# Performance work log

Hardware: AMD Instinct MI355X
Metric: run time of the kernel (lower is better)

## Reference

```python
import jax, jax.numpy as jnp
import numpy as np

D_MODEL = 1024
N_HEADS = 16
SEQ = 2048
BATCH = 2


def setup_inputs() -> dict:
    key = jax.random.key(0)
    ks = jax.random.split(key, 12)
    s = 1.0 / np.sqrt(D_MODEL)
    return {
        "q_input": jax.random.normal(ks[0], (BATCH, SEQ, D_MODEL), jnp.float32),
        "k_input": jax.random.normal(ks[1], (BATCH, SEQ, D_MODEL), jnp.float32),
        "v_input": jax.random.normal(ks[2], (BATCH, SEQ, D_MODEL), jnp.float32),
        "key_padding_mask": jnp.zeros((BATCH, SEQ), dtype=bool),
        "wq": jax.random.normal(ks[3], (D_MODEL, D_MODEL), jnp.float32) * s,
        "bq": jnp.zeros((D_MODEL,), jnp.float32),
        "wk": jax.random.normal(ks[4], (D_MODEL, D_MODEL), jnp.float32) * s,
        "bk": jnp.zeros((D_MODEL,), jnp.float32),
        "wv": jax.random.normal(ks[5], (D_MODEL, D_MODEL), jnp.float32) * s,
        "bv": jnp.zeros((D_MODEL,), jnp.float32),
        "wo": jax.random.normal(ks[6], (D_MODEL, D_MODEL), jnp.float32) * s,
        "bo": jnp.zeros((D_MODEL,), jnp.float32),
    }


def reference(q_input, k_input, v_input, key_padding_mask, wq, bq, wk, bk, wv, bv, wo, bo):
    B, Lq, _ = q_input.shape
    Lk = k_input.shape[1]
    d_head = D_MODEL // N_HEADS
    # torch Linear: x @ W.T + b
    Q = q_input @ wq.T + bq
    K = k_input @ wk.T + bk
    V = v_input @ wv.T + bv
    # [B, H, L, d_head]
    Qh = Q.reshape(B, Lq, N_HEADS, d_head).transpose(0, 2, 1, 3)
    Kh = K.reshape(B, Lk, N_HEADS, d_head).transpose(0, 2, 1, 3)
    Vh = V.reshape(B, Lk, N_HEADS, d_head).transpose(0, 2, 1, 3)
    scores = jnp.einsum("bhqd,bhkd->bhqk", Qh, Kh) / jnp.sqrt(jnp.float32(d_head))
    # causal mask (use_mask=True)
    causal = jnp.arange(Lk)[None, :] > jnp.arange(Lq)[:, None]  # [Lq, Lk]
    scores = jnp.where(causal[None, None], -jnp.inf, scores)
    # key padding mask [B,1,1,Lk]
    scores = jnp.where(key_padding_mask[:, None, None, :], -jnp.inf, scores)
    # module's global all-inf fallback (scalar condition)
    probs = jnp.where(
        jnp.all(jnp.isinf(scores)),
        jnp.full_like(scores, 1.0 / Lk),
        jax.nn.softmax(scores, axis=-1),
    )
    # dropout is identity in eval mode
    out = jnp.einsum("bhqk,bhkd->bhqd", probs, Vh)
    out = out.transpose(0, 2, 1, 3).reshape(B, Lq, D_MODEL)
    return out @ wo.T + bo
```

## Files before the change

kernel.cpp:

```cpp
#include <hip/hip_runtime.h>
#include <cstdint>
#include <cstddef>

#define DM   1024
#define HEADS 16
#define DH    64
#define SEQL  2048
#define BATCH 2
#define MTOT  (BATCH*SEQL)

typedef __attribute__((ext_vector_type(8))) short short8;
typedef __attribute__((ext_vector_type(4))) float floatx4;

__device__ __forceinline__ unsigned short f2bf(float f) {
  unsigned int u = __float_as_uint(f);
  u = (u + 0x7FFFu + ((u >> 16) & 1u)) >> 16;
  return (unsigned short)u;
}

__device__ __forceinline__ float exp2_fast(float x) {
#if __has_builtin(__builtin_amdgcn_exp2f)
  return __builtin_amdgcn_exp2f(x);
#else
  return exp2f(x);
#endif
}

__device__ __forceinline__ unsigned int cvt_pk_bf16(float lo, float hi) {
  unsigned int r;
  asm("v_cvt_pk_bf16_f32 %0, %1, %2" : "=v"(r) : "v"(lo), "v"(hi));
  return r;
}

__device__ __forceinline__ void async_ld16(const void* g, void* l) {
  __builtin_amdgcn_global_load_lds(
      (const __attribute__((address_space(1))) unsigned int*)g,
      (__attribute__((address_space(3))) unsigned int*)l, 16, 0, 0);
}

#define QSCALE 0.1803368801111204f

__global__ void cvt_all(const float* __restrict__ q, const float* __restrict__ k,
                        const float* __restrict__ v, const float* __restrict__ w0,
                        const float* __restrict__ w1, const float* __restrict__ w2,
                        const float* __restrict__ w3,
                        unsigned short* __restrict__ Xq, unsigned short* __restrict__ Xk,
                        unsigned short* __restrict__ Xv, unsigned short* __restrict__ W0,
                        unsigned short* __restrict__ W1, unsigned short* __restrict__ W2,
                        unsigned short* __restrict__ W3) {
  const int bid = blockIdx.x;
  const float* src; unsigned short* dst; int base;
  if (bid < 12288) {
    int seg = bid >> 12;
    base = (bid & 4095) * 1024;
    src = seg == 0 ? q : seg == 1 ? k : v;
    dst = seg == 0 ? Xq : seg == 1 ? Xk : Xv;
  } else {
    int b2 = bid - 12288;
    int seg = b2 >> 10;
    base = (b2 & 1023) * 1024;
    src = seg == 0 ? w0 : seg == 1 ? w1 : seg == 2 ? w2 : w3;
    dst = seg == 0 ? W0 : seg == 1 ? W1 : seg == 2 ? W2 : W3;
  }
  int i = base + threadIdx.x * 4;
  float4 vv = *(const float4*)(src + i);
  ushort4 o;
  o.x = f2bf(vv.x); o.y = f2bf(vv.y); o.z = f2bf(vv.z); o.w = f2bf(vv.w);
  *(ushort4*)(dst + i) = o;
}

__global__ __launch_bounds__(256, 3) void qkv_gemm(
    const unsigned short* Xq, const unsigned short* Xk, const unsigned short* Xv,
    const unsigned short* Wq, const unsigned short* Wk, const unsigned short* Wv,
    const float* bq, const float* bk, const float* bv,
    unsigned short* Qo, unsigned short* Ko, unsigned short* VTo) {
  __shared__ unsigned short As[128 * 64], Bs[128 * 64];
  const unsigned short *A, *Bw; const float* bias; unsigned short* Cout;
  if (blockIdx.z == 0)      { A = Xq; Bw = Wq; bias = bq; Cout = Qo; }
  else if (blockIdx.z == 1) { A = Xk; Bw = Wk; bias = bk; Cout = Ko; }
  else                      { A = Xv; Bw = Wv; bias = bv; Cout = VTo; }

  const int K = DM, N = DM;
  const int m0 = blockIdx.y * 128, n0 = blockIdx.x * 128;
  const int tid  = threadIdx.x;
  const int lane = tid & 63, wvi = tid >> 6;
  const int lq = lane & 15, quad = lane >> 4;
  const int wrow = wvi >> 1, wcol = wvi & 1;

  floatx4 acc[4][4];
  #pragma unroll
  for (int i = 0; i < 4; i++)
    #pragma unroll
    for (int j = 0; j < 4; j++)
      #pragma unroll
      for (int e = 0; e < 4; e++) acc[i][j][e] = 0.0f;

  for (int kt = 0; kt < K; kt += 64) {
    #pragma unroll
    for (int cc = 0; cc < 4; cc++) {
      int c = wvi + cc * 4;
      int e = c * 512 + lane * 8;
      int r = e >> 6, col = e & 63;
      async_ld16(A  + (size_t)(m0 + r) * K + kt + col, As + c * 512);
      async_ld16(Bw + (size_t)(n0 + r) * K + kt + col, Bs + c * 512);
    }
    __syncthreads();
    #pragma unroll
    for (int ks = 0; ks < 64; ks += 32) {
      short8 af[4], bf[4];
      #pragma unroll
      for (int i = 0; i < 4; i++)
        af[i] = *(const short8*)&As[(wrow * 64 + i * 16 + lq) * 64 + ks + quad * 8];
      #pragma unroll
      for (int j = 0; j < 4; j++)
        bf[j] = *(const short8*)&Bs[(wcol * 64 + j * 16 + lq) * 64 + ks + quad * 8];
      #pragma unroll
      for (int i = 0; i < 4; i++)
        #pragma unroll
        for (int j = 0; j < 4; j++)
          acc[i][j] = __builtin_amdgcn_mfma_f32_16x16x32_bf16(af[i], bf[j], acc[i][j], 0, 0, 0);
    }
    __syncthreads();
  }

  if (blockIdx.z == 2) {
    #pragma unroll
    for (int i = 0; i < 4; i++) {
      const int rowg = m0 + wrow * 64 + i * 16 + quad * 4;
      const int bb  = rowg >> 11;
      const int kt2 = (rowg & 2047) >> 6;
      const int k0  = rowg & 63;
      #pragma unroll
      for (int j = 0; j < 4; j++) {
        const int colg = n0 + wcol * 64 + j * 16 + lq;
        const int h2 = colg >> 6, d2 = colg & 63;
        const float bb_v = bias[colg];
        ushort4 w;
        w.x = f2bf(acc[i][j][0] + bb_v);
        w.y = f2bf(acc[i][j][1] + bb_v);
        w.z = f2bf(acc[i][j][2] + bb_v);
        w.w = f2bf(acc[i][j][3] + bb_v);
        *(ushort4*)(Cout + (size_t)((bb * HEADS + h2) * 32 + kt2) * 4096 + d2 * 64 + k0) = w;
      }
    }
  } else {
    const float oscale = (blockIdx.z == 0) ? QSCALE : 1.0f;
    #pragma unroll
    for (int i = 0; i < 4; i++) {
      #pragma unroll
      for (int j = 0; j < 4; j++) {
        int colg = n0 + wcol * 64 + j * 16 + lq;
        float bb = bias[colg];
        #pragma unroll
        for (int r = 0; r < 4; r++) {
          int rowg = m0 + wrow * 64 + i * 16 + quad * 4 + r;
          Cout[(size_t)rowg * N + colg] = f2bf((acc[i][j][r] + bb) * oscale);
        }
      }
    }
  }
}

__global__ __launch_bounds__(256, 4) void out_gemm(
    const unsigned short* __restrict__ A, const unsigned short* __restrict__ Bw,
    const float* __restrict__ bias, float* __restrict__ C) {
  __shared__ unsigned short As[64 * 64], Bs[128 * 64];
  const int K = DM, N = DM;
  const int m0 = blockIdx.y * 64, n0 = blockIdx.x * 128;
  const int tid  = threadIdx.x;
  const int lane = tid & 63, wvi = tid >> 6;
  const int lq = lane & 15, quad = lane >> 4;

  floatx4 acc[8];
  #pragma unroll
  for (int j = 0; j < 8; j++)
    #pragma unroll
    for (int e = 0; e < 4; e++) acc[j][e] = 0.0f;

  for (int kt = 0; kt < K; kt += 64) {
    #pragma unroll
    for (int cc = 0; cc < 2; cc++) {
      int c = wvi + cc * 4;
      int e = c * 512 + lane * 8;
      int r = e >> 6, col = e & 63;
      async_ld16(A + (size_t)(m0 + r) * K + kt + col, As + c * 512);
    }
    #pragma unroll
    for (int cc = 0; cc < 4; cc++) {
      int c = wvi + cc * 4;
      int e = c * 512 + lane * 8;
      int r = e >> 6, col = e & 63;
      async_ld16(Bw + (size_t)(n0 + r) * K + kt + col, Bs + c * 512);
    }
    __syncthreads();
    #pragma unroll
    for (int ks = 0; ks < 64; ks += 32) {
      const short8 af = *(const short8*)&As[(wvi * 16 + lq) * 64 + ks + quad * 8];
      #pragma unroll
      for (int j = 0; j < 8; j++) {
        const short8 bf = *(const short8*)&Bs[(j * 16 + lq) * 64 + ks + quad * 8];
        acc[j] = __builtin_amdgcn_mfma_f32_16x16x32_bf16(af, bf, acc[j], 0, 0, 0);
      }
    }
    __syncthreads();
  }

  #pragma unroll
  for (int j = 0; j < 8; j++) {
    const int colg = n0 + j * 16 + lq;
    const float bb = bias[colg];
    #pragma unroll
    for (int r = 0; r < 4; r++) {
      const int rowg = m0 + wvi * 16 + quad * 4 + r;
      C[(size_t)rowg * N + colg] = acc[j][r] + bb;
    }
  }
}

__global__ __launch_bounds__(256, 4) void attn_kernel(
    const unsigned short* __restrict__ Q, const unsigned short* __restrict__ K,
    const unsigned short* __restrict__ VT, const unsigned char* __restrict__ kpm,
    unsigned short* __restrict__ O) {
  __shared__ unsigned short Ks[64 * 72];
  __shared__ unsigned short VTs[64 * 72];
  __shared__ unsigned short Ps[4][16 * 72];

  const int bid = blockIdx.x;
  const int qt = 31 - (bid >> 5);
  const int bh = bid & 31;
  const int h = bh & 15, b = bh >> 4;
  const int tid = threadIdx.x, lane = tid & 63, wvi = tid >> 6;
  const int lq = lane & 15, quad = lane >> 4;
  const size_t bbase = (size_t)b * SEQL * DM;

  const int srow = tid >> 4;
  const int scol = (tid & 15) * 4;

  const unsigned short* kptr = K + bbase + (size_t)h * DH + (size_t)srow * DM + scol;
  const unsigned short* vptr = VT + (size_t)(b * HEADS + h) * 32 * 4096 + srow * 64 + scol;
  const unsigned char*  mptr = kpm + (size_t)b * SEQL + quad * 4;

  const unsigned short* Qrow = Q + bbase + (size_t)(qt * 64 + wvi * 16 + lq) * DM + h * DH;
  const short8 qf0 = *(const short8*)(Qrow + quad * 8);
  const short8 qf1 = *(const short8*)(Qrow + 32 + quad * 8);

  ushort4 kr[4], vr[4];
  unsigned int mr[4];
  #pragma unroll
  for (int j = 0; j < 4; j++) {
    kr[j] = *(const ushort4*)(kptr + (size_t)j * 16 * DM);
    vr[j] = *(const ushort4*)(vptr + j * 1024);
  }
  #pragma unroll
  for (int t = 0; t < 4; t++) mr[t] = *(const unsigned int*)(mptr + t * 16);
  kptr += (size_t)64 * DM; vptr += 4096; mptr += 64;

  floatx4 o[4];
  #pragma unroll
  for (int t = 0; t < 4; t++)
    #pragma unroll
    for (int e = 0; e < 4; e++) o[t][e] = 0.f;

  floatx4 lacc;
  #pragma unroll
  for (int e = 0; e < 4; e++) lacc[e] = 0.f;

  floatx4 zf;
  #pragma unroll
  for (int e = 0; e < 4; e++) zf[e] = 0.f;

  const unsigned short one_bf = 0x3F80;
  short8 ones8;
  #pragma unroll
  for (int e = 0; e < 8; e++) ones8[e] = (short)one_bf;

  const int qg = wvi * 16 + lq;

  auto tile_body = [&](bool diag, const unsigned int* mcur) {
    floatx4 st[4];
    #pragma unroll
    for (int t = 0; t < 4; t++) {
      const short8 a0 = *(const short8*)&Ks[(t * 16 + lq) * 72 + quad * 8];
      const short8 a1 = *(const short8*)&Ks[(t * 16 + lq) * 72 + 32 + quad * 8];
      st[t] = __builtin_amdgcn_mfma_f32_16x16x32_bf16(a0, qf0, zf, 0, 0, 0);
      st[t] = __builtin_amdgcn_mfma_f32_16x16x32_bf16(a1, qf1, st[t], 0, 0, 0);
    }

    float x[4][4];
    #pragma unroll
    for (int t = 0; t < 4; t++)
      #pragma unroll
      for (int r = 0; r < 4; r++) x[t][r] = st[t][r];

    if (__any((int)((mcur[0] | mcur[1] | mcur[2] | mcur[3]) != 0u))) {
      #pragma unroll
      for (int t = 0; t < 4; t++)
        #pragma unroll
        for (int r = 0; r < 4; r++)
          if ((mcur[t] >> (8 * r)) & 0xffu) x[t][r] = -1e33f;
    }
    if (diag) {
      #pragma unroll
      for (int t = 0; t < 4; t++)
        #pragma unroll
        for (int r = 0; r < 4; r++)
          if (t * 16 + quad * 4 + r > qg) x[t][r] = -1e33f;
    }

    #pragma unroll
    for (int t = 0; t < 4; t++)
      #pragma unroll
      for (int r = 0; r < 4; r++)
        x[t][r] = exp2_fast(x[t][r]);

    #pragma unroll
    for (int t = 0; t < 4; t++) {
      unsigned int p01 = cvt_pk_bf16(x[t][0], x[t][1]);
      unsigned int p23 = cvt_pk_bf16(x[t][2], x[t][3]);
      *(uint2*)&Ps[wvi][lq * 72 + t * 16 + quad * 4] = make_uint2(p01, p23);
    }

    const short8 pa0 = *(const short8*)&Ps[wvi][lq * 72 + quad * 8];
    const short8 pa1 = *(const short8*)&Ps[wvi][lq * 72 + 32 + quad * 8];
    #pragma unroll
    for (int t = 0; t < 4; t++) {
      const short8 b0 = *(const short8*)&VTs[(t * 16 + lq) * 72 + quad * 8];
      const short8 b1 = *(const short8*)&VTs[(t * 16 + lq) * 72 + 32 + quad * 8];
      o[t] = __builtin_amdgcn_mfma_f32_16x16x32_bf16(pa0, b0, o[t], 0, 0, 0);
      o[t] = __builtin_amdgcn_mfma_f32_16x16x32_bf16(pa1, b1, o[t], 0, 0, 0);
    }
    lacc = __builtin_amdgcn_mfma_f32_16x16x32_bf16(pa0, ones8, lacc, 0, 0, 0);
    lacc = __builtin_amdgcn_mfma_f32_16x16x32_bf16(pa1, ones8, lacc, 0, 0, 0);
  };

  for (int kt = 0; kt < qt; kt++) {
    __syncthreads();
    #pragma unroll
    for (int j = 0; j < 4; j++) {
      *(ushort4*)&Ks [(j * 16 + srow) * 72 + scol] = kr[j];
      *(ushort4*)&VTs[(j * 16 + srow) * 72 + scol] = vr[j];
    }
    unsigned int mcur[4];
    #pragma unroll
    for (int t = 0; t < 4; t++) mcur[t] = mr[t];
    __syncthreads();

    #pragma unroll
    for (int j = 0; j < 4; j++) {
      kr[j] = *(const ushort4*)(kptr + (size_t)j * 16 * DM);
      vr[j] = *(const ushort4*)(vptr + j * 1024);
    }
    #pragma unroll
    for (int t = 0; t < 4; t++) mr[t] = *(const unsigned int*)(mptr + t * 16);
    kptr += (size_t)64 * DM; vptr += 4096; mptr += 64;

    tile_body(false, mcur);
  }

  __syncthreads();
  #pragma unroll
  for (int j = 0; j < 4; j++) {
    *(ushort4*)&Ks [(j * 16 + srow) * 72 + scol] = kr[j];
    *(ushort4*)&VTs[(j * 16 + srow) * 72 + scol] = vr[j];
  }
  __syncthreads();
  tile_body(true, mr);

  float linv[4];
  #pragma unroll
  for (int r = 0; r < 4; r++) linv[r] = 1.0f / lacc[r];
  #pragma unroll
  for (int t = 0; t < 4; t++)
    #pragma unroll
    for (int r = 0; r < 4; r++) {
      const int rowg = qt * 64 + wvi * 16 + quad * 4 + r;
      const int colg = h * 64 + t * 16 + lq;
      O[bbase + (size_t)rowg * DM + colg] = f2bf(o[t][r] * linv[r]);
    }
}

extern "C" void kernel_launch(void* const* d_in, const int* in_sizes, int n_in,
                              void* d_out, int out_size, void* d_ws, size_t ws_size,
                              hipStream_t stream) {
  const float* qin = (const float*)d_in[0];
  const float* kin = (const float*)d_in[1];
  const float* vin = (const float*)d_in[2];
  const unsigned char* kpm = (const unsigned char*)d_in[3];
  const float* wq = (const float*)d_in[4];
  const float* bq = (const float*)d_in[5];
  const float* wk = (const float*)d_in[6];
  const float* bk = (const float*)d_in[7];
  const float* wv = (const float*)d_in[8];
  const float* bv = (const float*)d_in[9];
  const float* wo = (const float*)d_in[10];
  const float* bo = (const float*)d_in[11];

  const size_t XN = (size_t)MTOT * DM;
  const size_t WN = (size_t)DM * DM;
  unsigned short* Xq  = (unsigned short*)d_ws;
  unsigned short* Xk  = Xq  + XN;
  unsigned short* Xv  = Xk  + XN;
  unsigned short* Wqb = Xv  + XN;
  unsigned short* Wkb = Wqb + WN;
  unsigned short* Wvb = Wkb + WN;
  unsigned short* Wob = Wvb + WN;
  unsigned short* Qb  = Wob + WN;
  unsigned short* Kb  = Qb  + XN;
  unsigned short* VTg = Kb  + XN;
  unsigned short* Ob  = VTg + XN;

  cvt_all<<<dim3(16384), 256, 0, stream>>>(qin, kin, vin, wq, wk, wv, wo,
                                           Xq, Xk, Xv, Wqb, Wkb, Wvb, Wob);

  dim3 g1(DM / 128, MTOT / 128, 3);
  qkv_gemm<<<g1, 256, 0, stream>>>(Xq, Xk, Xv, Wqb, Wkb, Wvb, bq, bk, bv, Qb, Kb, VTg);

  attn_kernel<<<dim3(BATCH * HEADS * (SEQL / 64)), 256, 0, stream>>>(Qb, Kb, VTg, kpm, Ob);

  dim3 g2(DM / 128, MTOT / 64, 1);
  out_gemm<<<g2, 256, 0, stream>>>(Ob, Wob, bo, (float*)d_out);
}
```

Baseline: 222.7 us.

## Process two query tiles per attention block to reuse staged K/V tiles

Each attention block now covers 128 query rows, held as two 64-row groups per wave, instead of 64. Every K/V tile staged in shared memory feeds both groups. Causal masking is handled per group: on the second-to-last key tile the first group is on its diagonal, and on the last tile only the second group computes. This halves the global-to-LDS K/V traffic and the number of syncs per unit of work, at the cost of more registers (launch bounds lowered to 2), half as many blocks, and coarser load balance across the causal triangle.

```diff
diff --git a/kernel.cpp b/kernel.cpp
--- a/kernel.cpp
+++ b/kernel.cpp
@@ -217,16 +217,16 @@
   }
 }
 
-__global__ __launch_bounds__(256, 4) void attn_kernel(
+__global__ __launch_bounds__(256, 2) void attn_kernel(
     const unsigned short* __restrict__ Q, const unsigned short* __restrict__ K,
     const unsigned short* __restrict__ VT, const unsigned char* __restrict__ kpm,
     unsigned short* __restrict__ O) {
   __shared__ unsigned short Ks[64 * 72];
   __shared__ unsigned short VTs[64 * 72];
-  __shared__ unsigned short Ps[4][16 * 72];
+  __shared__ unsigned short Ps[4][2][16 * 72];
 
   const int bid = blockIdx.x;
-  const int qt = 31 - (bid >> 5);
+  const int qt = 15 - (bid >> 5);
   const int bh = bid & 31;
   const int h = bh & 15, b = bh >> 4;
   const int tid = threadIdx.x, lane = tid & 63, wvi = tid >> 6;
@@ -240,9 +240,14 @@
   const unsigned short* vptr = VT + (size_t)(b * HEADS + h) * 32 * 4096 + srow * 64 + scol;
   const unsigned char*  mptr = kpm + (size_t)b * SEQL + quad * 4;
 
-  const unsigned short* Qrow = Q + bbase + (size_t)(qt * 64 + wvi * 16 + lq) * DM + h * DH;
-  const short8 qf0 = *(const short8*)(Qrow + quad * 8);
-  const short8 qf1 = *(const short8*)(Qrow + 32 + quad * 8);
+  short8 qf[2][2];
+  #pragma unroll
+  for (int g = 0; g < 2; g++) {
+    const unsigned short* Qrow =
+        Q + bbase + (size_t)(qt * 128 + g * 64 + wvi * 16 + lq) * DM + h * DH;
+    qf[g][0] = *(const short8*)(Qrow + quad * 8);
+    qf[g][1] = *(const short8*)(Qrow + 32 + quad * 8);
+  }
 
   ushort4 kr[4], vr[4];
   unsigned int mr[4];
@@ -255,85 +260,113 @@
   for (int t = 0; t < 4; t++) mr[t] = *(const unsigned int*)(mptr + t * 16);
   kptr += (size_t)64 * DM; vptr += 4096; mptr += 64;
 
-  floatx4 o[4];
-  #pragma unroll
-  for (int t = 0; t < 4; t++)
-    #pragma unroll
-    for (int e = 0; e < 4; e++) o[t][e] = 0.f;
-
-  floatx4 lacc;
-  #pragma unroll
-  for (int e = 0; e < 4; e++) lacc[e] = 0.f;
+  floatx4 o[2][4];
+  floatx4 lacc[2];
+  #pragma unroll
+  for (int g = 0; g < 2; g++) {
+    #pragma unroll
+    for (int t = 0; t < 4; t++)
+      #pragma unroll
+      for (int e = 0; e < 4; e++) o[g][t][e] = 0.f;
+    #pragma unroll
+    for (int e = 0; e < 4; e++) lacc[g][e] = 0.f;
+  }
 
   floatx4 zf;
   #pragma unroll
   for (int e = 0; e < 4; e++) zf[e] = 0.f;
 
-  const unsigned short one_bf = 0x3F80;
   short8 ones8;
   #pragma unroll
-  for (int e = 0; e < 8; e++) ones8[e] = (short)one_bf;
+  for (int e = 0; e < 8; e++) ones8[e] = (short)0x3F80;
 
   const int qg = wvi * 16 + lq;
 
-  auto tile_body = [&](bool diag, const unsigned int* mcur) {
-    floatx4 st[4];
+  auto tile_body = [&](int m0, int m1, const unsigned int* mcur) {
+    floatx4 st[2][4];
     #pragma unroll
     for (int t = 0; t < 4; t++) {
       const short8 a0 = *(const short8*)&Ks[(t * 16 + lq) * 72 + quad * 8];
       const short8 a1 = *(const short8*)&Ks[(t * 16 + lq) * 72 + 32 + quad * 8];
-      st[t] = __builtin_amdgcn_mfma_f32_16x16x32_bf16(a0, qf0, zf, 0, 0, 0);
-      st[t] = __builtin_amdgcn_mfma_f32_16x16x32_bf16(a1, qf1, st[t], 0, 0, 0);
-    }
-
-    float x[4][4];
-    #pragma unroll
-    for (int t = 0; t < 4; t++)
-      #pragma unroll
-      for (int r = 0; r < 4; r++) x[t][r] = st[t][r];
-
-    if (__any((int)((mcur[0] | mcur[1] | mcur[2] | mcur[3]) != 0u))) {
+      if (m0 != 2) {
+        st[0][t] = __builtin_amdgcn_mfma_f32_16x16x32_bf16(a0, qf[0][0], zf, 0, 0, 0);
+        st[0][t] = __builtin_amdgcn_mfma_f32_16x16x32_bf16(a1, qf[0][1], st[0][t], 0, 0, 0);
+      }
+      st[1][t] = __builtin_amdgcn_mfma_f32_16x16x32_bf16(a0, qf[1][0], zf, 0, 0, 0);
+      st[1][t] = __builtin_amdgcn_mfma_f32_16x16x32_bf16(a1, qf[1][1], st[1][t], 0, 0, 0);
+    }
+
+    const bool any_pad =
+        __any((int)((mcur[0] | mcur[1] | mcur[2] | mcur[3]) != 0u));
+
+    #pragma unroll
+    for (int g = 0; g < 2; g++) {
+      if (g == 0 && m0 == 2) continue;
+      const int dmode = (g == 0) ? m0 : m1;
+      float x[4][4];
       #pragma unroll
       for (int t = 0; t < 4; t++)
         #pragma unroll
+        for (int r = 0; r < 4; r++) x[t][r] = st[g][t][r];
+
+      if (any_pad) {
+        #pragma unroll
+        for (int t = 0; t < 4; t++)
+          #pragma unroll
+          for (int r = 0; r < 4; r++)
+            if ((mcur[t] >> (8 * r)) & 0xffu) x[t][r] = -1e33f;
+      }
+      if (dmode == 1) {
+        #pragma unroll
+        for (int t = 0; t < 4; t++)
+          #pragma unroll
+          for (int r = 0; r < 4; r++)
+            if (t * 16 + quad * 4 + r > qg) x[t][r] = -1e33f;
+      }
+
+      #pragma unroll
+      for (int t = 0; t < 4; t++)
+        #pragma unroll
         for (int r = 0; r < 4; r++)
-          if ((mcur[t] >> (8 * r)) & 0xffu) x[t][r] = -1e33f;
-    }
-    if (diag) {
-      #pragma unroll
-      for (int t = 0; t < 4; t++)
-        #pragma unroll
-        for (int r = 0; r < 4; r++)
-          if (t * 16 + quad * 4 + r > qg) x[t][r] = -1e33f;
-    }
-
-    #pragma unroll
-    for (int t = 0; t < 4; t++)
-      #pragma unroll
-      for (int r = 0; r < 4; r++)
-        x[t][r] = exp2_fast(x[t][r]);
-
-    #pragma unroll
-    for (int t = 0; t < 4; t++) {
-      unsigned int p01 = cvt_pk_bf16(x[t][0], x[t][1]);
-      unsigned int p23 = cvt_pk_bf16(x[t][2], x[t][3]);
-      *(uint2*)&Ps[wvi][lq * 72 + t * 16 + quad * 4] = make_uint2(p01, p23);
-    }
-
-    const short8 pa0 = *(const short8*)&Ps[wvi][lq * 72 + quad * 8];
-    const short8 pa1 = *(const short8*)&Ps[wvi][lq * 72 + 32 + quad * 8];
+          x[t][r] = exp2_fast(x[t][r]);
+
+      #pragma unroll
+      for (int t = 0; t < 4; t++) {
+        unsigned int p01 = cvt_pk_bf16(x[t][0], x[t][1]);
+        unsigned int p23 = cvt_pk_bf16(x[t][2], x[t][3]);
+        *(uint2*)&Ps[wvi][g][lq * 72 + t * 16 + quad * 4] = make_uint2(p01, p23);
+      }
+    }
+
+    short8 pa[2][2];
+    if (m0 != 2) {
+      pa[0][0] = *(const short8*)&Ps[wvi][0][lq * 72 + quad * 8];
+      pa[0][1] = *(const short8*)&Ps[wvi][0][lq * 72 + 32 + quad * 8];
+    }
+    pa[1][0] = *(const short8*)&Ps[wvi][1][lq * 72 + quad * 8];
+    pa[1][1] = *(const short8*)&Ps[wvi][1][lq * 72 + 32 + quad * 8];
+
     #pragma unroll
     for (int t = 0; t < 4; t++) {
       const short8 b0 = *(const short8*)&VTs[(t * 16 + lq) * 72 + quad * 8];
       const short8 b1 = *(const short8*)&VTs[(t * 16 + lq) * 72 + 32 + quad * 8];
-      o[t] = __builtin_amdgcn_mfma_f32_16x16x32_bf16(pa0, b0, o[t], 0, 0, 0);
-      o[t] = __builtin_amdgcn_mfma_f32_16x16x32_bf16(pa1, b1, o[t], 0, 0, 0);
-    }
-    lacc = __builtin_amdgcn_mfma_f32_16x16x32_bf16(pa0, ones8, lacc, 0, 0, 0);
-    lacc = __builtin_amdgcn_mfma_f32_16x16x32_bf16(pa1, ones8, lacc, 0, 0, 0);
+      if (m0 != 2) {
+        o[0][t] = __builtin_amdgcn_mfma_f32_16x16x32_bf16(pa[0][0], b0, o[0][t], 0, 0, 0);
+        o[0][t] = __builtin_amdgcn_mfma_f32_16x16x32_bf16(pa[0][1], b1, o[0][t], 0, 0, 0);
+      }
+      o[1][t] = __builtin_amdgcn_mfma_f32_16x16x32_bf16(pa[1][0], b0, o[1][t], 0, 0, 0);
+      o[1][t] = __builtin_amdgcn_mfma_f32_16x16x32_bf16(pa[1][1], b1, o[1][t], 0, 0, 0);
+    }
+    if (m0 != 2) {
+      lacc[0] = __builtin_amdgcn_mfma_f32_16x16x32_bf16(pa[0][0], ones8, lacc[0], 0, 0, 0);
+      lacc[0] = __builtin_amdgcn_mfma_f32_16x16x32_bf16(pa[0][1], ones8, lacc[0], 0, 0, 0);
+    }
+    lacc[1] = __builtin_amdgcn_mfma_f32_16x16x32_bf16(pa[1][0], ones8, lacc[1], 0, 0, 0);
+    lacc[1] = __builtin_amdgcn_mfma_f32_16x16x32_bf16(pa[1][1], ones8, lacc[1], 0, 0, 0);
   };
 
-  for (int kt = 0; kt < qt; kt++) {
+  const int nkt = 2 * qt + 2;
+  for (int kt = 0; kt < nkt - 1; kt++) {
     __syncthreads();
     #pragma unroll
     for (int j = 0; j < 4; j++) {
@@ -354,7 +387,7 @@
     for (int t = 0; t < 4; t++) mr[t] = *(const unsigned int*)(mptr + t * 16);
     kptr += (size_t)64 * DM; vptr += 4096; mptr += 64;
 
-    tile_body(false, mcur);
+    tile_body(kt == nkt - 2 ? 1 : 0, 0, mcur);
   }
 
   __syncthreads();
@@ -364,19 +397,22 @@
     *(ushort4*)&VTs[(j * 16 + srow) * 72 + scol] = vr[j];
   }
   __syncthreads();
-  tile_body(true, mr);
-
-  float linv[4];
-  #pragma unroll
-  for (int r = 0; r < 4; r++) linv[r] = 1.0f / lacc[r];
-  #pragma unroll
-  for (int t = 0; t < 4; t++)
-    #pragma unroll
-    for (int r = 0; r < 4; r++) {
-      const int rowg = qt * 64 + wvi * 16 + quad * 4 + r;
-      const int colg = h * 64 + t * 16 + lq;
-      O[bbase + (size_t)rowg * DM + colg] = f2bf(o[t][r] * linv[r]);
-    }
+  tile_body(2, 1, mr);
+
+  #pragma unroll
+  for (int g = 0; g < 2; g++) {
+    float linv[4];
+    #pragma unroll
+    for (int r = 0; r < 4; r++) linv[r] = 1.0f / lacc[g][r];
+    #pragma unroll
+    for (int t = 0; t < 4; t++)
+      #pragma unroll
+      for (int r = 0; r < 4; r++) {
+        const int rowg = qt * 128 + g * 64 + wvi * 16 + quad * 4 + r;
+        const int colg = h * 64 + t * 16 + lq;
+        O[bbase + (size_t)rowg * DM + colg] = f2bf(o[g][t][r] * linv[r]);
+      }
+  }
 }
 
 extern "C" void kernel_launch(void* const* d_in, const int* in_sizes, int n_in,
@@ -415,7 +451,7 @@
   dim3 g1(DM / 128, MTOT / 128, 3);
   qkv_gemm<<<g1, 256, 0, stream>>>(Xq, Xk, Xv, Wqb, Wkb, Wvb, bq, bk, bv, Qb, Kb, VTg);
 
-  attn_kernel<<<dim3(BATCH * HEADS * (SEQL / 64)), 256, 0, stream>>>(Qb, Kb, VTg, kpm, Ob);
+  attn_kernel<<<dim3(BATCH * HEADS * (SEQL / 128)), 256, 0, stream>>>(Qb, Kb, VTg, kpm, Ob);
 
   dim3 g2(DM / 128, MTOT / 64, 1);
   out_gemm<<<g2, 256, 0, stream>>>(Ob, Wob, bo, (float*)d_out);
```

Measured after the change: 222.8 us. No clear change (+0.0%).

## Double-buffer K tile in LDS and load V fragments directly from global

Applied to the files above, without the earlier changes.

The attention kernel now keeps two K tiles in shared memory and synchronizes once per key tile instead of twice, with the next tile staged from registers while the current one is processed. V^T operand fragments and the padding mask are loaded straight from global memory into MFMA registers each iteration, so the V shared-memory buffer and its staging are removed. This cuts barriers and LDS traffic, but V loads are no longer prefetched one tile ahead, so their global latency may be exposed right before the PV MFMAs. The explicit diagonal-tile epilogue is folded into the main loop.

```diff
diff --git a/kernel.cpp b/kernel.cpp
--- a/kernel.cpp
+++ b/kernel.cpp
@@ -221,8 +221,7 @@
     const unsigned short* __restrict__ Q, const unsigned short* __restrict__ K,
     const unsigned short* __restrict__ VT, const unsigned char* __restrict__ kpm,
     unsigned short* __restrict__ O) {
-  __shared__ unsigned short Ks[64 * 72];
-  __shared__ unsigned short VTs[64 * 72];
+  __shared__ unsigned short Ks[2][64 * 72];
   __shared__ unsigned short Ps[4][16 * 72];
 
   const int bid = blockIdx.x;
@@ -236,32 +235,35 @@
   const int srow = tid >> 4;
   const int scol = (tid & 15) * 4;
 
-  const unsigned short* kptr = K + bbase + (size_t)h * DH + (size_t)srow * DM + scol;
-  const unsigned short* vptr = VT + (size_t)(b * HEADS + h) * 32 * 4096 + srow * 64 + scol;
-  const unsigned char*  mptr = kpm + (size_t)b * SEQL + quad * 4;
+  const unsigned short* kptr  = K + bbase + (size_t)h * DH + (size_t)srow * DM + scol;
+  const unsigned short* vbase = VT + (size_t)(b * HEADS + h) * 32 * 4096 + lq * 64 + quad * 8;
+  const unsigned char*  mbase = kpm + (size_t)b * SEQL + quad * 4;
 
   const unsigned short* Qrow = Q + bbase + (size_t)(qt * 64 + wvi * 16 + lq) * DM + h * DH;
   const short8 qf0 = *(const short8*)(Qrow + quad * 8);
   const short8 qf1 = *(const short8*)(Qrow + 32 + quad * 8);
 
-  ushort4 kr[4], vr[4];
-  unsigned int mr[4];
-  #pragma unroll
-  for (int j = 0; j < 4; j++) {
+  const int nkt = qt + 1;
+
+  ushort4 kr[4];
+  #pragma unroll
+  for (int j = 0; j < 4; j++)
     kr[j] = *(const ushort4*)(kptr + (size_t)j * 16 * DM);
-    vr[j] = *(const ushort4*)(vptr + j * 1024);
-  }
-  #pragma unroll
-  for (int t = 0; t < 4; t++) mr[t] = *(const unsigned int*)(mptr + t * 16);
-  kptr += (size_t)64 * DM; vptr += 4096; mptr += 64;
+  #pragma unroll
+  for (int j = 0; j < 4; j++)
+    *(ushort4*)&Ks[0][(j * 16 + srow) * 72 + scol] = kr[j];
+  if (nkt > 1) {
+    #pragma unroll
+    for (int j = 0; j < 4; j++)
+      kr[j] = *(const ushort4*)(kptr + (size_t)(64 + j * 16) * DM);
+  }
 
   floatx4 o[4];
+  floatx4 lacc;
   #pragma unroll
   for (int t = 0; t < 4; t++)
     #pragma unroll
     for (int e = 0; e < 4; e++) o[t][e] = 0.f;
-
-  floatx4 lacc;
   #pragma unroll
   for (int e = 0; e < 4; e++) lacc[e] = 0.f;
 
@@ -269,19 +271,46 @@
   #pragma unroll
   for (int e = 0; e < 4; e++) zf[e] = 0.f;
 
-  const unsigned short one_bf = 0x3F80;
   short8 ones8;
   #pragma unroll
-  for (int e = 0; e < 8; e++) ones8[e] = (short)one_bf;
+  for (int e = 0; e < 8; e++) ones8[e] = (short)0x3F80;
 
   const int qg = wvi * 16 + lq;
 
-  auto tile_body = [&](bool diag, const unsigned int* mcur) {
+  __syncthreads();
+
+  for (int kt = 0; kt < nkt; kt++) {
+    const int cur = kt & 1, nxt = cur ^ 1;
+
+    if (kt + 1 < nkt) {
+      #pragma unroll
+      for (int j = 0; j < 4; j++)
+        *(ushort4*)&Ks[nxt][(j * 16 + srow) * 72 + scol] = kr[j];
+    }
+    if (kt + 2 < nkt) {
+      #pragma unroll
+      for (int j = 0; j < 4; j++)
+        kr[j] = *(const ushort4*)(kptr + (size_t)((kt + 2) * 64 + j * 16) * DM);
+    }
+
+    short8 vf[4][2];
+    #pragma unroll
+    for (int t = 0; t < 4; t++) {
+      vf[t][0] = *(const short8*)(vbase + (size_t)kt * 4096 + t * 1024);
+      vf[t][1] = *(const short8*)(vbase + (size_t)kt * 4096 + t * 1024 + 32);
+    }
+    unsigned int mcur[4];
+    #pragma unroll
+    for (int t = 0; t < 4; t++)
+      mcur[t] = *(const unsigned int*)(mbase + kt * 64 + t * 16);
+
+    const bool diag = (kt == nkt - 1);
+
     floatx4 st[4];
     #pragma unroll
     for (int t = 0; t < 4; t++) {
-      const short8 a0 = *(const short8*)&Ks[(t * 16 + lq) * 72 + quad * 8];
-      const short8 a1 = *(const short8*)&Ks[(t * 16 + lq) * 72 + 32 + quad * 8];
+      const short8 a0 = *(const short8*)&Ks[cur][(t * 16 + lq) * 72 + quad * 8];
+      const short8 a1 = *(const short8*)&Ks[cur][(t * 16 + lq) * 72 + 32 + quad * 8];
       st[t] = __builtin_amdgcn_mfma_f32_16x16x32_bf16(a0, qf0, zf, 0, 0, 0);
       st[t] = __builtin_amdgcn_mfma_f32_16x16x32_bf16(a1, qf1, st[t], 0, 0, 0);
     }
@@ -324,47 +353,14 @@
     const short8 pa1 = *(const short8*)&Ps[wvi][lq * 72 + 32 + quad * 8];
     #pragma unroll
     for (int t = 0; t < 4; t++) {
-      const short8 b0 = *(const short8*)&VTs[(t * 16 + lq) * 72 + quad * 8];
-      const short8 b1 = *(const short8*)&VTs[(t * 16 + lq) * 72 + 32 + quad * 8];
-      o[t] = __builtin_amdgcn_mfma_f32_16x16x32_bf16(pa0, b0, o[t], 0, 0, 0);
-      o[t] = __builtin_amdgcn_mfma_f32_16x16x32_bf16(pa1, b1, o[t], 0, 0, 0);
+      o[t] = __builtin_amdgcn_mfma_f32_16x16x32_bf16(pa0, vf[t][0], o[t], 0, 0, 0);
+      o[t] = __builtin_amdgcn_mfma_f32_16x16x32_bf16(pa1, vf[t][1], o[t], 0, 0, 0);
     }
     lacc = __builtin_amdgcn_mfma_f32_16x16x32_bf16(pa0, ones8, lacc, 0, 0, 0);
     lacc = __builtin_amdgcn_mfma_f32_16x16x32_bf16(pa1, ones8, lacc, 0, 0, 0);
-  };
-
-  for (int kt = 0; kt < qt; kt++) {
+
     __syncthreads();
-    #pragma unroll
-    for (int j = 0; j < 4; j++) {
-      *(ushort4*)&Ks [(j * 16 + srow) * 72 + scol] = kr[j];
-      *(ushort4*)&VTs[(j * 16 + srow) * 72 + scol] = vr[j];
-    }
-    unsigned int mcur[4];
-    #pragma unroll
-    for (int t = 0; t < 4; t++) mcur[t] = mr[t];
-    __syncthreads();
-
-    #pragma unroll
-    for (int j = 0; j < 4; j++) {
-      kr[j] = *(const ushort4*)(kptr + (size_t)j * 16 * DM);
-      vr[j] = *(const ushort4*)(vptr + j * 1024);
-    }
-    #pragma unroll
-    for (int t = 0; t < 4; t++) mr[t] = *(const unsigned int*)(mptr + t * 16);
-    kptr += (size_t)64 * DM; vptr += 4096; mptr += 64;
-
-    tile_body(false, mcur);
-  }
-
-  __syncthreads();
-  #pragma unroll
-  for (int j = 0; j < 4; j++) {
-    *(ushort4*)&Ks [(j * 16 + srow) * 72 + scol] = kr[j];
-    *(ushort4*)&VTs[(j * 16 + srow) * 72 + scol] = vr[j];
-  }
-  __syncthreads();
-  tile_body(true, mr);
+  }
 
   float linv[4];
   #pragma unroll
```

After: 273.5 us. 22.8% more time.
